# Performance work log

Measured on AMD Instinct MI355X. Metric: run time of the kernel, lower is better.

The kernel has to match this reference:

```python
import jax, jax.numpy as jnp
import numpy as np

TAU = 0.5
K = 1024
EPS = 1e-5


def _bn(x, gamma=None, beta=None):
    # torch training-mode BatchNorm1d: biased batch stats over the batch dim
    mu = jnp.mean(x, axis=0)
    var = jnp.mean(jnp.square(x - mu), axis=0)
    xn = (x - mu) * jax.lax.rsqrt(var + EPS)
    if gamma is not None:
        xn = xn * gamma + beta
    return xn


def setup_inputs() -> dict:
    key = jax.random.key(0)
    ks = jax.random.split(key, 5)
    B, D, M, C = 128, 2048, 8192, 2048
    f = jax.random.normal(ks[0], (B, D), dtype=jnp.float32)
    w1 = jax.random.normal(ks[1], (M, D), dtype=jnp.float32) * 0.02
    w2 = jax.random.normal(ks[2], (M, M), dtype=jnp.float32) * 0.02
    w3 = jax.random.normal(ks[3], (C, M), dtype=jnp.float32) * 0.02
    return {
        "f": f,
        "w1": w1, "b1": jnp.zeros((M,), jnp.float32),
        "g1": jnp.ones((M,), jnp.float32), "be1": jnp.zeros((M,), jnp.float32),
        "w2": w2, "b2": jnp.zeros((M,), jnp.float32),
        "g2": jnp.ones((M,), jnp.float32), "be2": jnp.zeros((M,), jnp.float32),
        "w3": w3, "b3": jnp.zeros((C,), jnp.float32),
    }


def reference(f, w1, b1, g1, be1, w2, b2, g2, be2, w3, b3):
    # MLP head (dropout is identity in eval mode; BN uses batch statistics)
    h = jax.nn.relu(_bn(f @ w1.T + b1, g1, be1))
    h = jax.nn.relu(_bn(h @ w2.T + b2, g2, be2))
    logits = _bn(h @ w3.T + b3)  # final BatchNorm1d(affine=False)

    rng = jax.random.key(42)

    def step(carry, _):
        mask, z, key = carry
        key, sub = jax.random.split(key)
        g = jax.random.gumbel(sub, mask.shape, mask.dtype)
        mask = jax.nn.softmax((mask + g) / TAU, axis=1)  # soft gumbel-softmax
        z = jnp.maximum(mask, z)
        return (mask, z, key), None

    z0 = jnp.zeros_like(logits)
    (_, z, _), _ = jax.lax.scan(step, (logits, z0, rng), None, length=K)
    return z
```

## Files before the change

### kernel.cpp

```cpp
#include <hip/hip_runtime.h>
#include <stdint.h>


__device__ __forceinline__ uint32_t rotl32(uint32_t v, int r) {
  return (v << r) | (v >> (32 - r));
}

__device__ __forceinline__ void tf2x32(uint32_t k0, uint32_t k1,
                                       uint32_t x0, uint32_t x1,
                                       uint32_t& o0, uint32_t& o1) {
  uint32_t k2 = k0 ^ k1 ^ 0x1BD11BDAu;
  x0 += k0; x1 += k1;
#define TFR(r) { x0 += x1; x1 = rotl32(x1, (r)); x1 ^= x0; }
  TFR(13) TFR(15) TFR(26) TFR(6)   x0 += k1; x1 += k2 + 1u;
  TFR(17) TFR(29) TFR(16) TFR(24)  x0 += k2; x1 += k0 + 2u;
  TFR(13) TFR(15) TFR(26) TFR(6)   x0 += k0; x1 += k1 + 3u;
  TFR(17) TFR(29) TFR(16) TFR(24)  x0 += k1; x1 += k2 + 4u;
  TFR(13) TFR(15) TFR(26) TFR(6)   x0 += k2; x1 += k0 + 5u;
#undef TFR
  o0 = x0; o1 = x1;
}

constexpr uint32_t crotl(uint32_t v, int r) { return (v << r) | (v >> (32 - r)); }
struct U2 { uint32_t a, b; };
constexpr U2 ctf(uint32_t k0, uint32_t k1, uint32_t x0, uint32_t x1) {
  uint32_t k2 = k0 ^ k1 ^ 0x1BD11BDAu;
  x0 += k0; x1 += k1;
#define CTFR(r) { x0 += x1; x1 = crotl(x1, (r)); x1 ^= x0; }
  CTFR(13) CTFR(15) CTFR(26) CTFR(6)   x0 += k1; x1 += k2 + 1u;
  CTFR(17) CTFR(29) CTFR(16) CTFR(24)  x0 += k2; x1 += k0 + 2u;
  CTFR(13) CTFR(15) CTFR(26) CTFR(6)   x0 += k0; x1 += k1 + 3u;
  CTFR(17) CTFR(29) CTFR(16) CTFR(24)  x0 += k1; x1 += k2 + 4u;
  CTFR(13) CTFR(15) CTFR(26) CTFR(6)   x0 += k2; x1 += k0 + 5u;
#undef CTFR
  return {x0, x1};
}

struct KeyTab { uint32_t v[2052]; };
constexpr KeyTab make_keys() {
  KeyTab t{};
  uint32_t ka = 0u, kb = 42u;
  for (int k = 0; k < 1026; ++k) {
    U2 c0 = ctf(ka, kb, 0u, 0u);
    U2 c1 = ctf(ka, kb, 0u, 1u);
    t.v[2 * k]     = c1.a;
    t.v[2 * k + 1] = c1.b;
    ka = c0.a; kb = c0.b;
  }
  return t;
}
__constant__ KeyTab d_keys = make_keys();

__device__ __forceinline__ float gumbel_cc(uint32_t bits) {
  float u = __uint_as_float((bits >> 9) | 0x3f800000u) - 1.0f;
  u = fmaxf(u, 1.17549435e-38f);
  float l = __log2f(u);
  float t = __log2f(-l);
  return fmaf(-2.0f, t, 1.0575327458538905f);
}

#define BK 16

__global__ __launch_bounds__(256) void gemm_splitk(
    const float* __restrict__ A, const float* __restrict__ W,
    float* __restrict__ P, int K, int N, int kchunk)
{
  __shared__ float sA[BK][132];
  __shared__ float sW[BK][132];
  const int tid = threadIdx.x;
  const int n0 = blockIdx.x * 128;
  const int k0 = blockIdx.y * kchunk;
  const int tx = tid & 15;
  const int ty = tid >> 4;

  float acc[8][8];
#pragma unroll
  for (int i = 0; i < 8; i++)
#pragma unroll
    for (int j = 0; j < 8; j++) acc[i][j] = 0.f;

  for (int kt = k0; kt < k0 + kchunk; kt += BK) {
#pragma unroll
    for (int i = 0; i < 2; i++) {
      int q = tid * 2 + i;
      int row = q >> 2;
      int kk = (q & 3) * 4;
      float4 av = *(const float4*)(A + (size_t)row * K + kt + kk);
      sA[kk + 0][row] = av.x; sA[kk + 1][row] = av.y;
      sA[kk + 2][row] = av.z; sA[kk + 3][row] = av.w;
      float4 wv = *(const float4*)(W + (size_t)(n0 + row) * K + kt + kk);
      sW[kk + 0][row] = wv.x; sW[kk + 1][row] = wv.y;
      sW[kk + 2][row] = wv.z; sW[kk + 3][row] = wv.w;
    }
    __syncthreads();
#pragma unroll
    for (int kk = 0; kk < BK; kk++) {
      float a[8], w[8];
#pragma unroll
      for (int i = 0; i < 8; i++) a[i] = sA[kk][ty * 8 + i];
#pragma unroll
      for (int j = 0; j < 8; j++) w[j] = sW[kk][tx * 8 + j];
#pragma unroll
      for (int i = 0; i < 8; i++)
#pragma unroll
        for (int j = 0; j < 8; j++)
          acc[i][j] = fmaf(a[i], w[j], acc[i][j]);
    }
    __syncthreads();
  }

  float* Ps = P + (size_t)blockIdx.y * 128 * N;
#pragma unroll
  for (int i = 0; i < 8; i++) {
    int b = ty * 8 + i;
#pragma unroll
    for (int j = 0; j < 8; j += 4) {
      float4 v = make_float4(acc[i][j], acc[i][j + 1], acc[i][j + 2], acc[i][j + 3]);
      *(float4*)(Ps + (size_t)b * N + n0 + tx * 8 + j) = v;
    }
  }
}

template <int CPB>
__global__ __launch_bounds__(256) void bn_kernel(
    const float* __restrict__ P, int nsl, int N,
    const float* __restrict__ bias, const float* __restrict__ gamma,
    const float* __restrict__ beta, float* __restrict__ out, int relu)
{
  constexpr int R = 256 / CPB;
  constexpr int NR = 128 / R;
  const int cl = threadIdx.x % CPB;
  const int rg = threadIdx.x / CPB;
  const int c = blockIdx.x * CPB + cl;
  const int r0 = rg * NR;

  float bc = bias ? bias[c] : 0.f;
  float xs[NR];
  float s = 0.f, s2 = 0.f;
#pragma unroll
  for (int i = 0; i < NR; i++) {
    float x = bc;
    for (int t = 0; t < nsl; t++)
      x += P[((size_t)t * 128 + r0 + i) * N + c];
    xs[i] = x; s += x; s2 += x * x;
  }

  __shared__ float sh_s[R][CPB], sh_s2[R][CPB];
  sh_s[rg][cl] = s; sh_s2[rg][cl] = s2;
  __syncthreads();
  float S = 0.f, S2 = 0.f;
#pragma unroll
  for (int g = 0; g < R; g++) { S += sh_s[g][cl]; S2 += sh_s2[g][cl]; }

  float mu = S * (1.f / 128.f);
  float var = S2 * (1.f / 128.f) - mu * mu;
  float rstd = rsqrtf(var + 1e-5f);
  float ga = gamma ? gamma[c] : 1.f;
  float be = beta ? beta[c] : 0.f;
  float scale = rstd * ga;
  float shift = be - mu * scale;
#pragma unroll
  for (int i = 0; i < NR; i++) {
    float y = fmaf(xs[i], scale, shift);
    if (relu) y = fmaxf(y, 0.f);
    out[(size_t)(r0 + i) * N + c] = y;
  }
}

__global__ __launch_bounds__(256) void noise_kernel(
    float* __restrict__ nbuf, int k0, int T)
{
  const int kk  = blockIdx.x >> 7;
  const int row = blockIdx.x & 127;
  const int k   = k0 + kk;
  const uint32_t ka = d_keys.v[2 * k], kb = d_keys.v[2 * k + 1];
  const int c0 = threadIdx.x * 4;
  float* base = nbuf + (size_t)kk * 262144 + row * 2048;
  uint32_t b0, b1;
  float4 v;
  uint32_t idx = (uint32_t)(row * 2048 + c0);
  tf2x32(ka, kb, 0u, idx + 0u, b0, b1); v.x = gumbel_cc(b0 ^ b1);
  tf2x32(ka, kb, 0u, idx + 1u, b0, b1); v.y = gumbel_cc(b0 ^ b1);
  tf2x32(ka, kb, 0u, idx + 2u, b0, b1); v.z = gumbel_cc(b0 ^ b1);
  tf2x32(ka, kb, 0u, idx + 3u, b0, b1); v.w = gumbel_cc(b0 ^ b1);
  *(float4*)(base + c0) = v;
  idx += 1024u;
  tf2x32(ka, kb, 0u, idx + 0u, b0, b1); v.x = gumbel_cc(b0 ^ b1);
  tf2x32(ka, kb, 0u, idx + 1u, b0, b1); v.y = gumbel_cc(b0 ^ b1);
  tf2x32(ka, kb, 0u, idx + 2u, b0, b1); v.z = gumbel_cc(b0 ^ b1);
  tf2x32(ka, kb, 0u, idx + 3u, b0, b1); v.w = gumbel_cc(b0 ^ b1);
  *(float4*)(base + 1024 + c0) = v;
}

__global__ __launch_bounds__(1024) void scan_kernel(
    const float* __restrict__ nbuf, int T,
    const float* __restrict__ msrc, float* __restrict__ mdst,
    float* __restrict__ zst, float* __restrict__ zout,
    int first, int last)
{
  const int tid = threadIdx.x;
  const int row = blockIdx.x;
  const int wid = tid >> 6, lane = tid & 63;
  __shared__ float s_sum[2][16];
  const float cc = 2.8853900817779268f;
  const size_t off = (size_t)row * 2048 + tid * 2;

  float2 mv = *(const float2*)(msrc + off);
  float m0 = mv.x, m1 = mv.y;
  float z0 = 0.f, z1 = 0.f;
  if (!first) { float2 zv = *(const float2*)(zst + off); z0 = zv.x; z1 = zv.y; }

  const float2* np = (const float2*)(nbuf + off);
  float2 na = np[0];
  float2 nb = np[131072];

  for (int kk = 0; kk < T; kk += 2) {
    {
      float e0 = exp2f(fmaf(m0, cc, na.x));
      float e1 = exp2f(fmaf(m1, cc, na.y));
      float ss = e0 + e1;
#pragma unroll
      for (int o = 1; o < 64; o <<= 1) ss += __shfl_xor(ss, o, 64);
      if (lane == 0) s_sum[0][wid] = ss;
      if (kk + 2 < T) na = np[(size_t)(kk + 2) * 131072];
      __syncthreads();
      const float4* sp = (const float4*)&s_sum[0][0];
      float4 q0 = sp[0], q1 = sp[1], q2 = sp[2], q3 = sp[3];
      float S = (((q0.x + q0.y) + (q0.z + q0.w)) + ((q1.x + q1.y) + (q1.z + q1.w)))
              + (((q2.x + q2.y) + (q2.z + q2.w)) + ((q3.x + q3.y) + (q3.z + q3.w)));
      float r = 1.0f / S;
      m0 = e0 * r; m1 = e1 * r;
      z0 = fmaxf(z0, m0); z1 = fmaxf(z1, m1);
    }
    {
      float e0 = exp2f(fmaf(m0, cc, nb.x));
      float e1 = exp2f(fmaf(m1, cc, nb.y));
      float ss = e0 + e1;
#pragma unroll
      for (int o = 1; o < 64; o <<= 1) ss += __shfl_xor(ss, o, 64);
      if (lane == 0) s_sum[1][wid] = ss;
      if (kk + 3 < T) nb = np[(size_t)(kk + 3) * 131072];
      __syncthreads();
      const float4* sp = (const float4*)&s_sum[1][0];
      float4 q0 = sp[0], q1 = sp[1], q2 = sp[2], q3 = sp[3];
      float S = (((q0.x + q0.y) + (q0.z + q0.w)) + ((q1.x + q1.y) + (q1.z + q1.w)))
              + (((q2.x + q2.y) + (q2.z + q2.w)) + ((q3.x + q3.y) + (q3.z + q3.w)));
      float r = 1.0f / S;
      m0 = e0 * r; m1 = e1 * r;
      z0 = fmaxf(z0, m0); z1 = fmaxf(z1, m1);
    }
  }

  if (last) {
    *(float2*)(zout + off) = make_float2(z0, z1);
  } else {
    *(float2*)(mdst + off) = make_float2(m0, m1);
    *(float2*)(zst + off)  = make_float2(z0, z1);
  }
}

extern "C" void kernel_launch(void* const* d_in, const int* in_sizes, int n_in,
                              void* d_out, int out_size, void* d_ws, size_t ws_size,
                              hipStream_t stream)
{
  const float* f   = (const float*)d_in[0];
  const float* w1  = (const float*)d_in[1];
  const float* b1  = (const float*)d_in[2];
  const float* g1  = (const float*)d_in[3];
  const float* be1 = (const float*)d_in[4];
  const float* w2  = (const float*)d_in[5];
  const float* b2  = (const float*)d_in[6];
  const float* g2  = (const float*)d_in[7];
  const float* be2 = (const float*)d_in[8];
  const float* w3  = (const float*)d_in[9];
  const float* b3  = (const float*)d_in[10];
  float* out = (float*)d_out;

  float* h1     = (float*)d_ws;
  float* h2     = h1 + 1048576;
  float* logits = h2 + 1048576;
  float* P      = logits + 262144;

  const size_t need_big = (size_t)(2359296 + 8388608) * 4;
  const int s12 = (ws_size >= need_big) ? 8 : 4;
  const int s3  = (ws_size >= need_big) ? 32 : 16;

  dim3 blk(256);
  gemm_splitk<<<dim3(64, s12), blk, 0, stream>>>(f, w1, P, 2048, 8192, 2048 / s12);
  bn_kernel<64><<<dim3(128), blk, 0, stream>>>(P, s12, 8192, b1, g1, be1, h1, 1);
  gemm_splitk<<<dim3(64, s12), blk, 0, stream>>>(h1, w2, P, 8192, 8192, 8192 / s12);
  bn_kernel<64><<<dim3(128), blk, 0, stream>>>(P, s12, 8192, b2, g2, be2, h2, 1);
  gemm_splitk<<<dim3(16, s3), blk, 0, stream>>>(h2, w3, P, 8192, 2048, 8192 / s3);
  bn_kernel<32><<<dim3(64), blk, 0, stream>>>(P, s3, 2048, b3, nullptr, nullptr, logits, 0);

  float* mstate = h1;
  float* zstate = h1 + 262144;
  float* nbuf   = P;
  size_t avail_f = ws_size / 4 - 2359296;
  int T = (int)(avail_f / 262144);
  if (T > 1024) T = 1024;
  T &= ~1;
  for (int k0 = 0; k0 < 1024; ) {
    int t = T; if (t > 1024 - k0) t = 1024 - k0;
    t &= ~1;
    noise_kernel<<<dim3(t * 128), dim3(256), 0, stream>>>(nbuf, k0, t);
    const int first = (k0 == 0);
    const int lastc = (k0 + t >= 1024);
    scan_kernel<<<dim3(128), dim3(1024), 0, stream>>>(
        nbuf, t, first ? logits : mstate, mstate, zstate, out, first, lastc);
    k0 += t;
  }
}
```

Measured before the change: 2.143 ms.

## Shrink scan blocks to 4 waves with 8 elements/thread and DPP reduction

Rewrites the gumbel-softmax scan kernel to use 256 threads per row, each holding 8 columns, so the per-step block reduction needs only 4 wave partials and a cheaper barrier. The intra-wave sum uses DPP row shifts and broadcasts instead of shuffles, and exp2 and the reciprocal use the raw hardware builtins. Noise prefetch is deepened to four steps ahead. In exchange there is more register pressure per thread, less parallelism per row, and slightly lower-precision rcp and exp.

```diff
diff --git a/kernel.cpp b/kernel.cpp
--- a/kernel.cpp
+++ b/kernel.cpp
@@ -58,6 +58,17 @@
   float t = __log2f(-l);
   return fmaf(-2.0f, t, 1.0575327458538905f);
 }
+
+#if __has_builtin(__builtin_amdgcn_exp2f)
+#define EXP2F(x) __builtin_amdgcn_exp2f(x)
+#else
+#define EXP2F(x) exp2f(x)
+#endif
+#if __has_builtin(__builtin_amdgcn_rcpf)
+#define RCPF(x) __builtin_amdgcn_rcpf(x)
+#else
+#define RCPF(x) (1.0f / (x))
+#endif
 
 #define BK 16
 
@@ -192,7 +203,22 @@
   *(float4*)(base + 1024 + c0) = v;
 }
 
-__global__ __launch_bounds__(1024) void scan_kernel(
+template <int CTRL, int RMASK>
+__device__ __forceinline__ float dpp_addstep(float v) {
+  int t = __builtin_amdgcn_update_dpp(0, __float_as_int(v), CTRL, RMASK, 0xF, false);
+  return v + __int_as_float(t);
+}
+__device__ __forceinline__ float wave_sum_dpp(float p) {
+  p = dpp_addstep<0x111, 0xF>(p);
+  p = dpp_addstep<0x112, 0xF>(p);
+  p = dpp_addstep<0x114, 0xF>(p);
+  p = dpp_addstep<0x118, 0xF>(p);
+  p = dpp_addstep<0x142, 0xA>(p);
+  p = dpp_addstep<0x143, 0xC>(p);
+  return p;
+}
+
+__global__ __launch_bounds__(256) void scan_kernel(
     const float* __restrict__ nbuf, int T,
     const float* __restrict__ msrc, float* __restrict__ mdst,
     float* __restrict__ zst, float* __restrict__ zout,
@@ -201,61 +227,74 @@
   const int tid = threadIdx.x;
   const int row = blockIdx.x;
   const int wid = tid >> 6, lane = tid & 63;
-  __shared__ float s_sum[2][16];
+  __shared__ __align__(16) float s_sum[2][4];
   const float cc = 2.8853900817779268f;
-  const size_t off = (size_t)row * 2048 + tid * 2;
-
-  float2 mv = *(const float2*)(msrc + off);
-  float m0 = mv.x, m1 = mv.y;
-  float z0 = 0.f, z1 = 0.f;
-  if (!first) { float2 zv = *(const float2*)(zst + off); z0 = zv.x; z1 = zv.y; }
-
-  const float2* np = (const float2*)(nbuf + off);
-  float2 na = np[0];
-  float2 nb = np[131072];
-
-  for (int kk = 0; kk < T; kk += 2) {
-    {
-      float e0 = exp2f(fmaf(m0, cc, na.x));
-      float e1 = exp2f(fmaf(m1, cc, na.y));
-      float ss = e0 + e1;
-#pragma unroll
-      for (int o = 1; o < 64; o <<= 1) ss += __shfl_xor(ss, o, 64);
-      if (lane == 0) s_sum[0][wid] = ss;
-      if (kk + 2 < T) na = np[(size_t)(kk + 2) * 131072];
-      __syncthreads();
-      const float4* sp = (const float4*)&s_sum[0][0];
-      float4 q0 = sp[0], q1 = sp[1], q2 = sp[2], q3 = sp[3];
-      float S = (((q0.x + q0.y) + (q0.z + q0.w)) + ((q1.x + q1.y) + (q1.z + q1.w)))
-              + (((q2.x + q2.y) + (q2.z + q2.w)) + ((q3.x + q3.y) + (q3.z + q3.w)));
-      float r = 1.0f / S;
-      m0 = e0 * r; m1 = e1 * r;
-      z0 = fmaxf(z0, m0); z1 = fmaxf(z1, m1);
-    }
-    {
-      float e0 = exp2f(fmaf(m0, cc, nb.x));
-      float e1 = exp2f(fmaf(m1, cc, nb.y));
-      float ss = e0 + e1;
-#pragma unroll
-      for (int o = 1; o < 64; o <<= 1) ss += __shfl_xor(ss, o, 64);
-      if (lane == 0) s_sum[1][wid] = ss;
-      if (kk + 3 < T) nb = np[(size_t)(kk + 3) * 131072];
-      __syncthreads();
-      const float4* sp = (const float4*)&s_sum[1][0];
-      float4 q0 = sp[0], q1 = sp[1], q2 = sp[2], q3 = sp[3];
-      float S = (((q0.x + q0.y) + (q0.z + q0.w)) + ((q1.x + q1.y) + (q1.z + q1.w)))
-              + (((q2.x + q2.y) + (q2.z + q2.w)) + ((q3.x + q3.y) + (q3.z + q3.w)));
-      float r = 1.0f / S;
-      m0 = e0 * r; m1 = e1 * r;
-      z0 = fmaxf(z0, m0); z1 = fmaxf(z1, m1);
-    }
-  }
+  const size_t off = (size_t)row * 2048 + tid * 8;
+
+  float m0, m1, m2, m3, m4, m5, m6, m7;
+  float z0, z1, z2, z3, z4, z5, z6, z7;
+  {
+    float4 a = *(const float4*)(msrc + off);
+    float4 b = *(const float4*)(msrc + off + 4);
+    m0 = a.x; m1 = a.y; m2 = a.z; m3 = a.w;
+    m4 = b.x; m5 = b.y; m6 = b.z; m7 = b.w;
+  }
+  if (first) {
+    z0 = z1 = z2 = z3 = z4 = z5 = z6 = z7 = 0.f;
+  } else {
+    float4 a = *(const float4*)(zst + off);
+    float4 b = *(const float4*)(zst + off + 4);
+    z0 = a.x; z1 = a.y; z2 = a.z; z3 = a.w;
+    z4 = b.x; z5 = b.y; z6 = b.z; z7 = b.w;
+  }
+
+  const float* nrow = nbuf + off;
+  float4 A0, A1, B0, B1, C0, C1, D0, D1;
+  { const float4* q = (const float4*)(nrow);                      A0 = q[0]; A1 = q[1]; }
+  { const float4* q = (const float4*)(nrow + 262144);             B0 = q[0]; B1 = q[1]; }
+  { const float4* q = (const float4*)(nrow + 2 * 262144);         C0 = q[0]; C1 = q[1]; }
+  { const float4* q = (const float4*)(nrow + 3 * 262144);         D0 = q[0]; D1 = q[1]; }
+
+#define STEP(N0, N1, KK, SLOT)                                               \
+  {                                                                          \
+    float e0 = EXP2F(fmaf(m0, cc, N0.x)), e1 = EXP2F(fmaf(m1, cc, N0.y));    \
+    float e2 = EXP2F(fmaf(m2, cc, N0.z)), e3 = EXP2F(fmaf(m3, cc, N0.w));    \
+    float e4 = EXP2F(fmaf(m4, cc, N1.x)), e5 = EXP2F(fmaf(m5, cc, N1.y));    \
+    float e6 = EXP2F(fmaf(m6, cc, N1.z)), e7 = EXP2F(fmaf(m7, cc, N1.w));    \
+    float p = ((e0 + e1) + (e2 + e3)) + ((e4 + e5) + (e6 + e7));             \
+    p = wave_sum_dpp(p);                                                     \
+    if (lane == 63) s_sum[SLOT][wid] = p;                                    \
+    if ((KK) + 4 < T) {                                                      \
+      const float4* q = (const float4*)(nrow + (size_t)((KK) + 4) * 262144); \
+      N0 = q[0]; N1 = q[1];                                                  \
+    }                                                                        \
+    __syncthreads();                                                         \
+    float4 sv = *(const float4*)&s_sum[SLOT][0];                             \
+    float r = RCPF((sv.x + sv.y) + (sv.z + sv.w));                           \
+    m0 = e0 * r; m1 = e1 * r; m2 = e2 * r; m3 = e3 * r;                      \
+    m4 = e4 * r; m5 = e5 * r; m6 = e6 * r; m7 = e7 * r;                      \
+    z0 = fmaxf(z0, m0); z1 = fmaxf(z1, m1);                                  \
+    z2 = fmaxf(z2, m2); z3 = fmaxf(z3, m3);                                  \
+    z4 = fmaxf(z4, m4); z5 = fmaxf(z5, m5);                                  \
+    z6 = fmaxf(z6, m6); z7 = fmaxf(z7, m7);                                  \
+  }
+
+  for (int kk = 0; kk < T; kk += 4) {
+    STEP(A0, A1, kk + 0, 0)
+    STEP(B0, B1, kk + 1, 1)
+    STEP(C0, C1, kk + 2, 0)
+    STEP(D0, D1, kk + 3, 1)
+  }
+#undef STEP
 
   if (last) {
-    *(float2*)(zout + off) = make_float2(z0, z1);
+    *(float4*)(zout + off)     = make_float4(z0, z1, z2, z3);
+    *(float4*)(zout + off + 4) = make_float4(z4, z5, z6, z7);
   } else {
-    *(float2*)(mdst + off) = make_float2(m0, m1);
-    *(float2*)(zst + off)  = make_float2(z0, z1);
+    *(float4*)(mdst + off)     = make_float4(m0, m1, m2, m3);
+    *(float4*)(mdst + off + 4) = make_float4(m4, m5, m6, m7);
+    *(float4*)(zst + off)      = make_float4(z0, z1, z2, z3);
+    *(float4*)(zst + off + 4)  = make_float4(z4, z5, z6, z7);
   }
 }
 
@@ -299,14 +338,14 @@
   size_t avail_f = ws_size / 4 - 2359296;
   int T = (int)(avail_f / 262144);
   if (T > 1024) T = 1024;
-  T &= ~1;
+  T &= ~3;
   for (int k0 = 0; k0 < 1024; ) {
     int t = T; if (t > 1024 - k0) t = 1024 - k0;
-    t &= ~1;
+    t &= ~3;
     noise_kernel<<<dim3(t * 128), dim3(256), 0, stream>>>(nbuf, k0, t);
     const int first = (k0 == 0);
     const int lastc = (k0 + t >= 1024);
-    scan_kernel<<<dim3(128), dim3(1024), 0, stream>>>(
+    scan_kernel<<<dim3(128), dim3(256), 0, stream>>>(
         nbuf, t, first ? logits : mstate, mstate, zstate, out, first, lastc);
     k0 += t;
   }
```

After: 1.841 ms. -14.1%, faster.
